# Optimization experiments

Measured on AMD Instinct MI355X. Metric: run time of the kernel, lower is better.

Reference implementation:

```python
import jax, jax.numpy as jnp
import numpy as np
import math

B, S, D, H = 2, 2048, 1024, 16
DH = D // H          # 64 head dim
BLK = 64             # SpargeAttn block size
TOPK = 0.5           # fraction of KV blocks kept per query block
NEG = -1e9


def setup_inputs() -> dict:
    key = jax.random.key(0)
    ks = jax.random.split(key, 8)
    s = 0.02
    return {
        "inputs": jax.random.normal(ks[0], (B, S, D), dtype=jnp.float32),
        "ln_g": jnp.ones((D,), jnp.float32),
        "ln_b": jnp.zeros((D,), jnp.float32),
        "Wq": jax.random.normal(ks[1], (D, D), jnp.float32) * s,
        "bq": jnp.zeros((D,), jnp.float32),
        "Wk": jax.random.normal(ks[2], (D, D), jnp.float32) * s,
        "bk": jnp.zeros((D,), jnp.float32),
        "Wv": jax.random.normal(ks[3], (D, D), jnp.float32) * s,
        "bv": jnp.zeros((D,), jnp.float32),
        "Wo": jax.random.normal(ks[4], (D, D), jnp.float32) * s,
        "bo": jnp.zeros((D,), jnp.float32),
    }


def _sparse_topk_attn(q, k, v):
    # q,k,v: [B,H,S,DH]. Block-mean-similarity top-k sparse causal attention
    # (SpargeAttn spas_sage2_attn_meansim_topk, fp32 reference semantics).
    nb = S // BLK
    qm = q.reshape(B, H, nb, BLK, DH).mean(3)          # [B,H,nb,DH]
    km = k.reshape(B, H, nb, BLK, DH).mean(3)
    sim = jnp.einsum('bhqd,bhkd->bhqk', qm, km)        # block similarity
    cblk = jnp.tril(jnp.ones((nb, nb), bool))          # causal block mask
    sim = jnp.where(cblk, sim, NEG)
    kk = max(1, int(math.ceil(TOPK * nb)))
    _, idx = jax.lax.top_k(sim, kk)                    # [B,H,nb,kk]
    blk = jax.nn.one_hot(idx, nb, dtype=jnp.float32).sum(-2) > 0  # [B,H,nb,nb]
    blk = (blk & cblk) | jnp.eye(nb, dtype=bool)       # keep diagonal block
    tok_mask = jnp.repeat(jnp.repeat(blk, BLK, axis=2), BLK, axis=3)  # [B,H,S,S]
    tok_mask = tok_mask & jnp.tril(jnp.ones((S, S), bool))
    scores = jnp.einsum('bhid,bhjd->bhij', q, k) / jnp.float32(math.sqrt(DH))
    scores = jnp.where(tok_mask, scores, NEG)
    p = jax.nn.softmax(scores, axis=-1)
    return jnp.einsum('bhij,bhjd->bhid', p, v)


def reference(inputs, ln_g, ln_b, Wq, bq, Wk, bk, Wv, bv, Wo, bo):
    # pre-norm LayerNorm
    mu = inputs.mean(-1, keepdims=True)
    var = inputs.var(-1, keepdims=True)
    x = (inputs - mu) * jax.lax.rsqrt(var + 1e-5) * ln_g + ln_b
    # QKV projections -> [B,H,S,DH]
    q = (x @ Wq + bq).reshape(B, S, H, DH).transpose(0, 2, 1, 3)
    k = (x @ Wk + bk).reshape(B, S, H, DH).transpose(0, 2, 1, 3)
    v = (x @ Wv + bv).reshape(B, S, H, DH).transpose(0, 2, 1, 3)
    ctx = _sparse_topk_attn(q, k, v)
    ctx = ctx.transpose(0, 2, 1, 3).reshape(B, S, D)
    return ctx @ Wo + bo
```

## Files before the change

kernel.cpp:

```cpp
#include <hip/hip_runtime.h>
#include <stdint.h>

#define DEV static __device__ __forceinline__

typedef __attribute__((ext_vector_type(8))) short s16x8;
typedef __attribute__((ext_vector_type(4))) float f32x4;

constexpr int Bdim = 2, Sdim = 2048, Ddim = 1024, Hdim = 16, DH = 64;
constexpr int Mrows = Bdim * Sdim;
constexpr int NB = 32;
constexpr int SEL_STRIDE = 18;

constexpr size_t OFF_XB    = 0;
constexpr size_t OFF_WTQKV = OFF_XB    + (size_t)Mrows*Ddim*2;
constexpr size_t OFF_WOT   = OFF_WTQKV + (size_t)3072*1024*2;
constexpr size_t OFF_QKV   = OFF_WOT   + (size_t)1024*1024*2;
constexpr size_t OFF_CTX   = OFF_QKV   + (size_t)Mrows*3072*2;
constexpr size_t OFF_XM    = OFF_CTX   + (size_t)Mrows*Ddim*2;
constexpr size_t OFF_QM    = OFF_XM    + (size_t)64*1024*4;
constexpr size_t OFF_KM    = OFF_QM    + (size_t)64*1024*4;
constexpr size_t OFF_BIASQ = OFF_KM    + (size_t)64*1024*4;
constexpr size_t OFF_SEL   = OFF_BIASQ + (size_t)3072*4;
constexpr size_t OFF_PART  = OFF_SEL   + (size_t)1024*SEL_STRIDE*4;

DEV float bf2f(unsigned short u){ union{unsigned int i; float f;} x; x.i = ((unsigned int)u)<<16; return x.f; }
DEV unsigned short f2bf(float f){ union{float f; unsigned int i;} x; x.f=f;
  unsigned int r = x.i + 0x7fffu + ((x.i>>16)&1u); return (unsigned short)(r>>16); }

DEV void gload16(const unsigned short* g, unsigned short* l){
  __builtin_amdgcn_global_load_lds(
      (__attribute__((address_space(1))) void*)(void*)g,
      (__attribute__((address_space(3))) void*)l, 16, 0, 0);
}

DEV float dppmax_step(float x, int v){ union{float f; int i;} a, b; a.f=x; b.i=v; return fmaxf(a.f,b.f); }
DEV float rowmax16(float x){
  union{float f; int i;} u;
  u.f = x; x = dppmax_step(x, __builtin_amdgcn_update_dpp(u.i,u.i,0xB1,0xF,0xF,true));
  u.f = x; x = dppmax_step(x, __builtin_amdgcn_update_dpp(u.i,u.i,0x4E,0xF,0xF,true));
  u.f = x; x = dppmax_step(x, __builtin_amdgcn_update_dpp(u.i,u.i,0x141,0xF,0xF,true));
  u.f = x; x = dppmax_step(x, __builtin_amdgcn_update_dpp(u.i,u.i,0x140,0xF,0xF,true));
  return x;
}

__global__ __launch_bounds__(256) void ln_kernel(const float* __restrict__ inp,
                                                 const float* __restrict__ gam,
                                                 const float* __restrict__ bet,
                                                 unsigned short* __restrict__ xb){
  const int row = blockIdx.x, t = threadIdx.x;
  __shared__ float red[8];
  const float4 v = ((const float4*)(inp + (size_t)row*Ddim))[t];
  float s  = v.x + v.y + v.z + v.w;
  float s2 = v.x*v.x + v.y*v.y + v.z*v.z + v.w*v.w;
#pragma unroll
  for (int mk=32; mk>=1; mk>>=1){ s += __shfl_xor(s, mk); s2 += __shfl_xor(s2, mk); }
  if ((t&63)==0){ red[t>>6] = s; red[4+(t>>6)] = s2; }
  __syncthreads();
  s  = red[0]+red[1]+red[2]+red[3];
  s2 = red[4]+red[5]+red[6]+red[7];
  const float mu  = s * (1.f/Ddim);
  const float var = s2 * (1.f/Ddim) - mu*mu;
  const float rs  = rsqrtf(var + 1e-5f);
  const float4 gv = ((const float4*)gam)[t];
  const float4 bv = ((const float4*)bet)[t];
  float o0 = (v.x-mu)*rs*gv.x + bv.x;
  float o1 = (v.y-mu)*rs*gv.y + bv.y;
  float o2 = (v.z-mu)*rs*gv.z + bv.z;
  float o3 = (v.w-mu)*rs*gv.w + bv.w;
  uint2 u;
  u.x = (unsigned int)f2bf(o0) | ((unsigned int)f2bf(o1)<<16);
  u.y = (unsigned int)f2bf(o2) | ((unsigned int)f2bf(o3)<<16);
  ((uint2*)(xb + (size_t)row*Ddim))[t] = u;
}

__global__ __launch_bounds__(256) void xm_kernel(const float* __restrict__ inp,
                                                 const float* __restrict__ gam,
                                                 const float* __restrict__ bet,
                                                 float* __restrict__ xm){
  const int blk = blockIdx.x, t = threadIdx.x;
  const int w = t>>6, lane = t&63;
  __shared__ float part[4][1024];
  float4 gv[4], bv[4];
#pragma unroll
  for (int p=0;p<4;++p){ gv[p] = ((const float4*)gam)[lane + 64*p];
                         bv[p] = ((const float4*)bet)[lane + 64*p]; }
  float ax[4][4];
#pragma unroll
  for (int p=0;p<4;++p)
#pragma unroll
    for (int c=0;c<4;++c) ax[p][c]=0.f;
  for (int rr=0; rr<16; ++rr){
    const int row = blk*64 + w*16 + rr;
    const float4* rp = (const float4*)(inp + (size_t)row*Ddim);
    float4 v[4]; float s=0.f, s2=0.f;
#pragma unroll
    for (int p=0;p<4;++p){
      v[p] = rp[lane + 64*p];
      s  += v[p].x+v[p].y+v[p].z+v[p].w;
      s2 += v[p].x*v[p].x+v[p].y*v[p].y+v[p].z*v[p].z+v[p].w*v[p].w;
    }
#pragma unroll
    for (int mk=32; mk>=1; mk>>=1){ s += __shfl_xor(s,mk); s2 += __shfl_xor(s2,mk); }
    const float mu = s*(1.f/Ddim);
    const float var = s2*(1.f/Ddim) - mu*mu;
    const float rs = rsqrtf(var + 1e-5f);
#pragma unroll
    for (int p=0;p<4;++p){
      ax[p][0] += (v[p].x-mu)*rs*gv[p].x + bv[p].x;
      ax[p][1] += (v[p].y-mu)*rs*gv[p].y + bv[p].y;
      ax[p][2] += (v[p].z-mu)*rs*gv[p].z + bv[p].z;
      ax[p][3] += (v[p].w-mu)*rs*gv[p].w + bv[p].w;
    }
  }
#pragma unroll
  for (int p=0;p<4;++p){
    float4 o; o.x=ax[p][0]; o.y=ax[p][1]; o.z=ax[p][2]; o.w=ax[p][3];
    ((float4*)&part[w][0])[lane + 64*p] = o;
  }
  __syncthreads();
  float4 r0 = ((float4*)&part[0][0])[t];
  float4 r1 = ((float4*)&part[1][0])[t];
  float4 r2 = ((float4*)&part[2][0])[t];
  float4 r3 = ((float4*)&part[3][0])[t];
  float4 o;
  o.x = (r0.x+r1.x+r2.x+r3.x)*(1.f/64);
  o.y = (r0.y+r1.y+r2.y+r3.y)*(1.f/64);
  o.z = (r0.z+r1.z+r2.z+r3.z)*(1.f/64);
  o.w = (r0.w+r1.w+r2.w+r3.w)*(1.f/64);
  ((float4*)(xm + (size_t)blk*Ddim))[t] = o;
}

__global__ __launch_bounds__(256) void wtrans4_kernel(const float* __restrict__ Wq,
                                                      const float* __restrict__ Wk,
                                                      const float* __restrict__ Wv,
                                                      const float* __restrict__ Wo,
                                                      unsigned short* __restrict__ wtqkv,
                                                      unsigned short* __restrict__ wot){
  __shared__ float tile[32][33];
  const int z = blockIdx.z;
  const float* W = (z==0)?Wq:(z==1)?Wk:(z==2)?Wv:Wo;
  unsigned short* Wt = (z<3) ? (wtqkv + (size_t)z*1024*1024) : wot;
  const int n0 = blockIdx.x*32, k0 = blockIdx.y*32;
  const int t = threadIdx.x, r = t>>5, c = t&31;
#pragma unroll
  for (int i=0;i<4;++i) tile[r+8*i][c] = W[(size_t)(k0 + r + 8*i)*1024 + n0 + c];
  __syncthreads();
#pragma unroll
  for (int i=0;i<4;++i) Wt[(size_t)(n0 + r + 8*i)*1024 + k0 + c] = f2bf(tile[c][r+8*i]);
}

__global__ void biascat_kernel(const float* __restrict__ bq, const float* __restrict__ bk,
                               const float* __restrict__ bv, float* __restrict__ outb){
  int i = blockIdx.x*256 + threadIdx.x;
  float v = (i<1024) ? bq[i] : (i<2048 ? bk[i-1024] : bv[i-2048]);
  outb[i] = v;
}

__global__ __launch_bounds__(256) void qmkm_part(const float* __restrict__ xm,
    const float* __restrict__ Wq, const float* __restrict__ Wk,
    float* __restrict__ part){
  const int c  = blockIdx.x*256 + threadIdx.x;
  const int rg = blockIdx.y >> 3, ks = blockIdx.y & 7;
  const int z  = blockIdx.z;
  const float* W = z ? Wk : Wq;
  const int r0 = rg*16, k0 = ks*128;
  float acc[16];
#pragma unroll
  for (int r=0;r<16;++r) acc[r]=0.f;
  for (int k=0;k<128;k+=4){
    const float wv0 = W[(size_t)(k0+k  )*1024 + c];
    const float wv1 = W[(size_t)(k0+k+1)*1024 + c];
    const float wv2 = W[(size_t)(k0+k+2)*1024 + c];
    const float wv3 = W[(size_t)(k0+k+3)*1024 + c];
#pragma unroll
    for (int r=0;r<16;++r){
      const float4 xv = *(const float4*)&xm[(size_t)(r0+r)*1024 + k0 + k];
      acc[r] = fmaf(xv.w, wv3, fmaf(xv.z, wv2, fmaf(xv.y, wv1, fmaf(xv.x, wv0, acc[r]))));
    }
  }
  float* dst = part + (((size_t)z*8 + ks)*64 + r0)*1024 + c;
#pragma unroll
  for (int r=0;r<16;++r) dst[(size_t)r*1024] = acc[r];
}

__global__ __launch_bounds__(256) void qmkm_reduce(const float* __restrict__ part,
    const float* __restrict__ bq, const float* __restrict__ bk,
    float* __restrict__ qm, float* __restrict__ km){
  const int idx = blockIdx.x*256 + threadIdx.x;
  const int z = blockIdx.y;
  const int c = idx & 1023, r = idx >> 10;
  const float* p = part + ((size_t)z*8*64*1024) + (size_t)r*1024 + c;
  float s = 0.f;
#pragma unroll
  for (int ks=0; ks<8; ++ks) s += p[(size_t)ks*64*1024];
  s += z ? bk[c] : bq[c];
  (z ? km : qm)[(size_t)r*1024 + c] = s;
}

__global__ __launch_bounds__(256) void topk_kernel(const float* __restrict__ qm,
                                                   const float* __restrict__ km,
                                                   int* __restrict__ sel){
  const int bhq = blockIdx.x;
  const int qb = bhq & 31, h = (bhq>>5) & 15, b = bhq >> 9;
  const int t = threadIdx.x;
  __shared__ float sim[32];
  __shared__ int keep[32];
  const int kb = t>>3, l8 = t&7;
  float acc = 0.f;
  if (kb <= qb){
    const float* qv = qm + (size_t)(b*32 + qb)*1024 + h*64;
    const float* kv = km + (size_t)(b*32 + kb)*1024 + h*64;
#pragma unroll
    for (int d=0; d<8; ++d) acc += qv[l8*8+d] * kv[l8*8+d];
  }
  acc += __shfl_xor(acc,1); acc += __shfl_xor(acc,2); acc += __shfl_xor(acc,4);
  if (l8==0) sim[kb] = (kb<=qb) ? acc : -1e30f;
  __syncthreads();
  if (t < 32){
    int k2 = t; int ok = 0;
    if (k2 <= qb){
      float sv = sim[k2]; int rank = 0;
      for (int j=0;j<=qb;++j){
        float sj = sim[j];
        rank += (sj > sv) || (sj == sv && j < k2);
      }
      ok = (rank < 16) || (k2 == qb);
    }
    keep[t] = ok;
  }
  __syncthreads();
  if (t == 0){
    int* dstp = sel + (size_t)bhq * SEL_STRIDE;
    int c = 0;
    for (int j=0;j<32;++j) if (keep[j]) dstp[1+c++] = j;
    dstp[0] = c;
  }
}

template<int OUT_BF16>
__global__ __launch_bounds__(256) void gemm_bt(const unsigned short* __restrict__ A,
                                               const unsigned short* __restrict__ Bt,
                                               const float* __restrict__ bias,
                                               void* __restrict__ C, int N){
  constexpr int K = 1024;
  __shared__ unsigned short ldsA[128*32];
  __shared__ unsigned short ldsB[128*32];
  const int t = threadIdx.x, lane = t & 63, wid = t >> 6;
  const int wr = wid >> 1, wc = wid & 1;
  const int rl = lane & 15, g = lane >> 4;

  const int nbx = gridDim.x;
  const int nwg = nbx * gridDim.y;
  const int id  = blockIdx.y * nbx + blockIdx.x;
  const int nid = (id & 7) * (nwg >> 3) + (id >> 3);
  const int m0 = (nid / nbx) * 128, n0 = (nid % nbx) * 128;

  const f32x4 ZERO4 = {0.f,0.f,0.f,0.f};
  f32x4 acc[4][4];
#pragma unroll
  for (int i=0;i<4;++i)
#pragma unroll
    for (int j=0;j<4;++j) acc[i][j] = ZERO4;

  const int slot0 = wid*128 + lane, slot1 = slot0 + 64;
  const int sr0 = slot0>>2, sc0 = slot0&3;
  const int sr1 = slot1>>2, sc1 = slot1&3;
  const unsigned short* A0 = A  + (size_t)(m0 + sr0)*K + (sc0 ^ ((sr0>>1)&3))*8;
  const unsigned short* A1 = A  + (size_t)(m0 + sr1)*K + (sc1 ^ ((sr1>>1)&3))*8;
  const unsigned short* B0 = Bt + (size_t)(n0 + sr0)*K + (sc0 ^ ((sr0>>1)&3))*8;
  const unsigned short* B1 = Bt + (size_t)(n0 + sr1)*K + (sc1 ^ ((sr1>>1)&3))*8;
  unsigned short* dA0 = ldsA + (wid*2+0)*512;
  unsigned short* dA1 = ldsA + (wid*2+1)*512;
  unsigned short* dB0 = ldsB + (wid*2+0)*512;
  unsigned short* dB1 = ldsB + (wid*2+1)*512;

  for (int k0=0; k0<K; k0+=32){
    __syncthreads();
    gload16(A0 + k0, dA0);
    gload16(A1 + k0, dA1);
    gload16(B0 + k0, dB0);
    gload16(B1 + k0, dB1);
    __syncthreads();
    s16x8 af[4], bfr[4];
#pragma unroll
    for (int mi=0;mi<4;++mi){
      int row = wr*64 + mi*16 + rl;
      af[mi] = *(const s16x8*)((char*)ldsA + row*64 + ((g ^ ((row>>1)&3))<<4));
    }
#pragma unroll
    for (int ni=0;ni<4;++ni){
      int row = wc*64 + ni*16 + rl;
      bfr[ni] = *(const s16x8*)((char*)ldsB + row*64 + ((g ^ ((row>>1)&3))<<4));
    }
#pragma unroll
    for (int mi=0;mi<4;++mi)
#pragma unroll
      for (int ni=0;ni<4;++ni)
        acc[mi][ni] = __builtin_amdgcn_mfma_f32_16x16x32_bf16(af[mi], bfr[ni], acc[mi][ni], 0,0,0);
  }

  const int r4 = g*4;
#pragma unroll
  for (int mi=0;mi<4;++mi){
#pragma unroll
    for (int ni=0;ni<4;++ni){
      int col = n0 + wc*64 + ni*16 + rl;
      float bb = bias[col];
#pragma unroll
      for (int e=0;e<4;++e){
        int row = m0 + wr*64 + mi*16 + r4 + e;
        float v = acc[mi][ni][e] + bb;
        if (OUT_BF16) ((unsigned short*)C)[(size_t)row*N + col] = f2bf(v);
        else          ((float*)C)[(size_t)row*N + col] = v;
      }
    }
  }
}

__global__ __launch_bounds__(256) void attn_kernel(const unsigned short* __restrict__ qkv,
                                                   const int* __restrict__ sel,
                                                   unsigned short* __restrict__ ctx){
  const int id = blockIdx.x;
  const int xcd = id & 7, jj = id >> 3;
  const int bh = xcd + 8*(jj/24);
  const int tau = jj % 24;
  const int h = bh & 15, b = bh >> 4;
  int qbl[2]; int nq;
  if (tau < 8){ qbl[0]=tau; qbl[1]=15-tau; nq=2; }
  else        { qbl[0]=tau+8; qbl[1]=0;    nq=1; }

  const int t = threadIdx.x, wid = t >> 6, lane = t & 63;
  const int rl = lane & 15, g = lane >> 4, r4 = g*4;

  __shared__ unsigned short K_s[2][64*64];
  __shared__ unsigned short V_s[2][80*64];
  __shared__ unsigned short P_s[4][16*64];

  for (int i=t; i<1024; i+=256){
    int r = 64 + (i>>6), c = i&63;
    unsigned short val = (r==64) ? (unsigned short)0x3F80 : (unsigned short)0;
    V_s[0][r*64+c] = val; V_s[1][r*64+c] = val;
  }

  const int jst = t >> 2, cq = t & 3;
  const unsigned short* kvbase = qkv + (size_t)(b*Sdim + jst)*3072 + h*DH;
  const int kwb0 = jst*128 + (((cq*2  ) ^ (jst&7))<<4);
  const int kwb1 = jst*128 + (((cq*2+1) ^ (jst&7))<<4);
  const f32x4 ZERO4 = {0.f,0.f,0.f,0.f};

  for (int iq=0; iq<nq; ++iq){
    const int qb = qbl[iq];
    const int* selrow = sel + (size_t)(((b*Hdim)+h)*NB + qb) * SEL_STRIDE;
    const int ns = selrow[0];

    const int qrow = b*Sdim + qb*64 + wid*16 + rl;
    const unsigned short* qbase = qkv + (size_t)qrow*3072 + h*DH;
    s16x8 qa[2];
#pragma unroll
    for (int kk=0; kk<2; ++kk){
      s16x8 raw = *(const s16x8*)(qbase + kk*32 + g*8);
      s16x8 qq;
#pragma unroll
      for (int e=0;e<8;++e) qq[e] = (short)f2bf(bf2f((unsigned short)raw[e]) * 0.125f);
      qa[kk] = qq;
    }

    f32x4 o[5];
    float m_r[4];
#pragma unroll
    for (int f=0; f<5; ++f) o[f] = ZERO4;
#pragma unroll
    for (int e=0;e<4;++e) m_r[e] = -3.0e38f;

    __syncthreads();

    int kb = selrow[1];
    s16x8 kr0, kr1, vr0, vr1;
    {
      const unsigned short* p = kvbase + (size_t)kb*64*3072;
      kr0 = *(const s16x8*)(p + 1024 + cq*16);
      kr1 = *(const s16x8*)(p + 1024 + cq*16 + 8);
      vr0 = *(const s16x8*)(p + 2048 + cq*16);
      vr1 = *(const s16x8*)(p + 2048 + cq*16 + 8);
    }

    for (int it=0; it<ns; ++it){
      const int buf = it & 1;
      unsigned short* Kw = &K_s[buf][0];
      unsigned short* Vw = &V_s[buf][0];
      *(s16x8*)((char*)Kw + kwb0) = kr0;
      *(s16x8*)((char*)Kw + kwb1) = kr1;
#pragma unroll
      for (int e=0;e<8;++e){
        int d1 = cq*16 + e, d2 = d1 + 8;
        int sw1 = (d1&7) ^ ((d1>>3)&7);
        int sw2 = (d2&7) ^ ((d2>>3)&7);
        *(unsigned short*)((char*)Vw + d1*128 + ((2*jst) ^ (sw1<<4))) = (unsigned short)vr0[e];
        *(unsigned short*)((char*)Vw + d2*128 + ((2*jst) ^ (sw2<<4))) = (unsigned short)vr1[e];
      }
      const int kbcur = kb;
      if (it+1 < ns){
        kb = selrow[2+it];
        const unsigned short* p = kvbase + (size_t)kb*64*3072;
        kr0 = *(const s16x8*)(p + 1024 + cq*16);
        kr1 = *(const s16x8*)(p + 1024 + cq*16 + 8);
        vr0 = *(const s16x8*)(p + 2048 + cq*16);
        vr1 = *(const s16x8*)(p + 2048 + cq*16 + 8);
      }
      __syncthreads();

      f32x4 sf[4];
#pragma unroll
      for (int f=0;f<4;++f) sf[f] = ZERO4;
#pragma unroll
      for (int kk=0;kk<2;++kk){
#pragma unroll
        for (int f=0;f<4;++f){
          int jr = f*16 + rl;
          s16x8 kf = *(const s16x8*)((char*)Kw + jr*128 + (((kk*4+g) ^ (jr&7))<<4));
          sf[f] = __builtin_amdgcn_mfma_f32_16x16x32_bf16(qa[kk], kf, sf[f], 0,0,0);
        }
      }
      if (kbcur == qb){
#pragma unroll
        for (int f=0;f<4;++f)
#pragma unroll
          for (int e=0;e<4;++e){
            int key = f*16 + rl;
            int qr  = wid*16 + r4 + e;
            if (key > qr) sf[f][e] = -1e9f;
          }
      }
      float alpha[4];
#pragma unroll
      for (int e=0;e<4;++e){
        float mx = fmaxf(fmaxf(sf[0][e], sf[1][e]), fmaxf(sf[2][e], sf[3][e]));
        mx = rowmax16(mx);
        float mn = fmaxf(m_r[e], mx);
        alpha[e] = __expf(m_r[e] - mn);
        m_r[e] = mn;
#pragma unroll
        for (int f=0;f<4;++f) sf[f][e] = __expf(sf[f][e] - mn);
      }
#pragma unroll
      for (int f=0;f<5;++f)
#pragma unroll
        for (int e=0;e<4;++e) o[f][e] = o[f][e] * alpha[e];

      char* Pw = (char*)&P_s[wid][0];
#pragma unroll
      for (int f=0;f<4;++f)
#pragma unroll
        for (int e=0;e<4;++e){
          int i_ = r4 + e;
          int sw = (i_&7) ^ (i_>>3);
          *(unsigned short*)(Pw + i_*128 + ((2*(f*16+rl)) ^ (sw<<4))) = f2bf(sf[f][e]);
        }

#pragma unroll
      for (int kk=0;kk<2;++kk){
        int swp = (rl&7) ^ (rl>>3);
        s16x8 pa = *(const s16x8*)(Pw + rl*128 + (((kk*4+g) ^ swp)<<4));
#pragma unroll
        for (int f=0;f<5;++f){
          int dr = f*16 + rl;
          int swv = (dr&7) ^ ((dr>>3)&7);
          s16x8 vf = *(const s16x8*)((char*)Vw + dr*128 + (((kk*4+g) ^ swv)<<4));
          o[f] = __builtin_amdgcn_mfma_f32_16x16x32_bf16(pa, vf, o[f], 0,0,0);
        }
      }
    }

    float l_e[4];
#pragma unroll
    for (int e=0;e<4;++e) l_e[e] = __shfl(o[4][e], lane & 48);
#pragma unroll
    for (int f=0;f<4;++f)
#pragma unroll
      for (int e=0;e<4;++e){
        int row = b*Sdim + qb*64 + wid*16 + r4 + e;
        int col = h*DH + f*16 + rl;
        ctx[(size_t)row*Ddim + col] = f2bf(o[f][e] / l_e[e]);
      }
  }
}

extern "C" void kernel_launch(void* const* d_in, const int* in_sizes, int n_in,
                              void* d_out, int out_size, void* d_ws, size_t ws_size,
                              hipStream_t stream){
  (void)in_sizes; (void)n_in; (void)out_size; (void)ws_size;
  const float* inp  = (const float*)d_in[0];
  const float* ln_g = (const float*)d_in[1];
  const float* ln_b = (const float*)d_in[2];
  const float* Wq   = (const float*)d_in[3];
  const float* bq   = (const float*)d_in[4];
  const float* Wk   = (const float*)d_in[5];
  const float* bk   = (const float*)d_in[6];
  const float* Wv   = (const float*)d_in[7];
  const float* bv   = (const float*)d_in[8];
  const float* Wo   = (const float*)d_in[9];
  const float* bo   = (const float*)d_in[10];

  char* ws = (char*)d_ws;
  unsigned short* xb    = (unsigned short*)(ws + OFF_XB);
  unsigned short* wtqkv = (unsigned short*)(ws + OFF_WTQKV);
  unsigned short* wot   = (unsigned short*)(ws + OFF_WOT);
  unsigned short* qkvb  = (unsigned short*)(ws + OFF_QKV);
  unsigned short* ctx   = (unsigned short*)(ws + OFF_CTX);
  float* xm   = (float*)(ws + OFF_XM);
  float* qm   = (float*)(ws + OFF_QM);
  float* km   = (float*)(ws + OFF_KM);
  float* bqkv = (float*)(ws + OFF_BIASQ);
  int*   sel  = (int*)(ws + OFF_SEL);
  float* part = (float*)(ws + OFF_PART);

  ln_kernel<<<Mrows, 256, 0, stream>>>(inp, ln_g, ln_b, xb);
  xm_kernel<<<64, 256, 0, stream>>>(inp, ln_g, ln_b, xm);
  wtrans4_kernel<<<dim3(32,32,4), 256, 0, stream>>>(Wq, Wk, Wv, Wo, wtqkv, wot);
  biascat_kernel<<<12, 256, 0, stream>>>(bq, bk, bv, bqkv);
  qmkm_part<<<dim3(4,32,2), 256, 0, stream>>>(xm, Wq, Wk, part);
  qmkm_reduce<<<dim3(256,2), 256, 0, stream>>>(part, bq, bk, qm, km);
  topk_kernel<<<1024, 256, 0, stream>>>(qm, km, sel);
  gemm_bt<1><<<dim3(24,32), 256, 0, stream>>>(xb, wtqkv, bqkv, (void*)qkvb, 3072);
  attn_kernel<<<768, 256, 0, stream>>>(qkvb, sel, ctx);
  gemm_bt<0><<<dim3(8,32), 256, 0, stream>>>(ctx, wot, bo, d_out, 1024);
}
```

Baseline: 164.2 us.

## Transpose attention score layout to keep P in registers; deepen GEMM K-tile

The attention kernel now computes S^T so that each lane holds one query row. Row max and sum then need only two cross-lane shuffles, and the softmax row sum is accumulated explicitly instead of through a ones-column in V. P is packed to bf16 with v_cvt_pk and redistributed through ds_bpermute rather than round-tripping through LDS, which removes the P_s buffer and the extra V column of MFMAs. Separately, the GEMM K-tile doubles to 64 with a new swizzle, halving barrier count per K, at the cost of more LDS per block.

```diff
diff --git a/kernel.cpp b/kernel.cpp
--- a/kernel.cpp
+++ b/kernel.cpp
@@ -33,14 +33,10 @@
       (__attribute__((address_space(3))) void*)l, 16, 0, 0);
 }
 
-DEV float dppmax_step(float x, int v){ union{float f; int i;} a, b; a.f=x; b.i=v; return fmaxf(a.f,b.f); }
-DEV float rowmax16(float x){
-  union{float f; int i;} u;
-  u.f = x; x = dppmax_step(x, __builtin_amdgcn_update_dpp(u.i,u.i,0xB1,0xF,0xF,true));
-  u.f = x; x = dppmax_step(x, __builtin_amdgcn_update_dpp(u.i,u.i,0x4E,0xF,0xF,true));
-  u.f = x; x = dppmax_step(x, __builtin_amdgcn_update_dpp(u.i,u.i,0x141,0xF,0xF,true));
-  u.f = x; x = dppmax_step(x, __builtin_amdgcn_update_dpp(u.i,u.i,0x140,0xF,0xF,true));
-  return x;
+DEV unsigned int cvtpk(float a, float b){
+  unsigned int r;
+  asm("v_cvt_pk_bf16_f32 %0, %1, %2" : "=v"(r) : "v"(a), "v"(b));
+  return r;
 }
 
 __global__ __launch_bounds__(256) void ln_kernel(const float* __restrict__ inp,
@@ -243,8 +239,8 @@
                                                const float* __restrict__ bias,
                                                void* __restrict__ C, int N){
   constexpr int K = 1024;
-  __shared__ unsigned short ldsA[128*32];
-  __shared__ unsigned short ldsB[128*32];
+  __shared__ unsigned short ldsA[128*64];
+  __shared__ unsigned short ldsB[128*64];
   const int t = threadIdx.x, lane = t & 63, wid = t >> 6;
   const int wr = wid >> 1, wc = wid & 1;
   const int rl = lane & 15, g = lane >> 4;
@@ -262,41 +258,42 @@
 #pragma unroll
     for (int j=0;j<4;++j) acc[i][j] = ZERO4;
 
-  const int slot0 = wid*128 + lane, slot1 = slot0 + 64;
-  const int sr0 = slot0>>2, sc0 = slot0&3;
-  const int sr1 = slot1>>2, sc1 = slot1&3;
-  const unsigned short* A0 = A  + (size_t)(m0 + sr0)*K + (sc0 ^ ((sr0>>1)&3))*8;
-  const unsigned short* A1 = A  + (size_t)(m0 + sr1)*K + (sc1 ^ ((sr1>>1)&3))*8;
-  const unsigned short* B0 = Bt + (size_t)(n0 + sr0)*K + (sc0 ^ ((sr0>>1)&3))*8;
-  const unsigned short* B1 = Bt + (size_t)(n0 + sr1)*K + (sc1 ^ ((sr1>>1)&3))*8;
-  unsigned short* dA0 = ldsA + (wid*2+0)*512;
-  unsigned short* dA1 = ldsA + (wid*2+1)*512;
-  unsigned short* dB0 = ldsB + (wid*2+0)*512;
-  unsigned short* dB1 = ldsB + (wid*2+1)*512;
-
-  for (int k0=0; k0<K; k0+=32){
+  const unsigned short* Ap[4]; const unsigned short* Bp[4];
+  unsigned short* dA[4]; unsigned short* dB[4];
+  const int csrc = (lane & 7) ^ (lane >> 3);
+#pragma unroll
+  for (int i=0;i<4;++i){
+    const int row_i = (wid*4+i)*8 + (lane>>3);
+    Ap[i] = A  + (size_t)(m0 + row_i)*K + csrc*8;
+    Bp[i] = Bt + (size_t)(n0 + row_i)*K + csrc*8;
+    dA[i] = ldsA + (wid*4+i)*512;
+    dB[i] = ldsB + (wid*4+i)*512;
+  }
+
+  for (int k0=0; k0<K; k0+=64){
     __syncthreads();
-    gload16(A0 + k0, dA0);
-    gload16(A1 + k0, dA1);
-    gload16(B0 + k0, dB0);
-    gload16(B1 + k0, dB1);
+#pragma unroll
+    for (int i=0;i<4;++i){ gload16(Ap[i] + k0, dA[i]); gload16(Bp[i] + k0, dB[i]); }
     __syncthreads();
-    s16x8 af[4], bfr[4];
-#pragma unroll
-    for (int mi=0;mi<4;++mi){
-      int row = wr*64 + mi*16 + rl;
-      af[mi] = *(const s16x8*)((char*)ldsA + row*64 + ((g ^ ((row>>1)&3))<<4));
-    }
-#pragma unroll
-    for (int ni=0;ni<4;++ni){
-      int row = wc*64 + ni*16 + rl;
-      bfr[ni] = *(const s16x8*)((char*)ldsB + row*64 + ((g ^ ((row>>1)&3))<<4));
-    }
-#pragma unroll
-    for (int mi=0;mi<4;++mi)
-#pragma unroll
-      for (int ni=0;ni<4;++ni)
-        acc[mi][ni] = __builtin_amdgcn_mfma_f32_16x16x32_bf16(af[mi], bfr[ni], acc[mi][ni], 0,0,0);
+#pragma unroll
+    for (int kk=0;kk<2;++kk){
+      s16x8 af[4], bfr[4];
+#pragma unroll
+      for (int mi=0;mi<4;++mi){
+        int row = wr*64 + mi*16 + rl;
+        af[mi] = *(const s16x8*)((char*)ldsA + row*128 + (((kk*4+g) ^ (rl&7))<<4));
+      }
+#pragma unroll
+      for (int ni=0;ni<4;++ni){
+        int row = wc*64 + ni*16 + rl;
+        bfr[ni] = *(const s16x8*)((char*)ldsB + row*128 + (((kk*4+g) ^ (rl&7))<<4));
+      }
+#pragma unroll
+      for (int mi=0;mi<4;++mi)
+#pragma unroll
+        for (int ni=0;ni<4;++ni)
+          acc[mi][ni] = __builtin_amdgcn_mfma_f32_16x16x32_bf16(af[mi], bfr[ni], acc[mi][ni], 0,0,0);
+    }
   }
 
   const int r4 = g*4;
@@ -330,31 +327,31 @@
   else        { qbl[0]=tau+8; qbl[1]=0;    nq=1; }
 
   const int t = threadIdx.x, wid = t >> 6, lane = t & 63;
-  const int rl = lane & 15, g = lane >> 4, r4 = g*4;
-
-  __shared__ unsigned short K_s[2][64*64];
-  __shared__ unsigned short V_s[2][80*64];
-  __shared__ unsigned short P_s[4][16*64];
-
-  for (int i=t; i<1024; i+=256){
-    int r = 64 + (i>>6), c = i&63;
-    unsigned short val = (r==64) ? (unsigned short)0x3F80 : (unsigned short)0;
-    V_s[0][r*64+c] = val; V_s[1][r*64+c] = val;
-  }
+  const int rl = lane & 15, g = lane >> 4;
+  const int q_local = wid*16 + rl;
+
+  __shared__ unsigned short K_s[2][4096];
+  __shared__ unsigned short V_s[2][4096];
 
   const int jst = t >> 2, cq = t & 3;
-  const unsigned short* kvbase = qkv + (size_t)(b*Sdim + jst)*3072 + h*DH;
+  const int r2 = t >> 3, dq = t & 7;
+  const unsigned short* kbase = qkv + (size_t)(b*Sdim + jst)*3072 + 1024 + h*DH + cq*16;
+  const unsigned short* vbase = qkv + (size_t)(b*Sdim + 2*r2)*3072 + 2048 + h*DH + dq*8;
   const int kwb0 = jst*128 + (((cq*2  ) ^ (jst&7))<<4);
   const int kwb1 = jst*128 + (((cq*2+1) ^ (jst&7))<<4);
   const f32x4 ZERO4 = {0.f,0.f,0.f,0.f};
+
+  const int src0 = (rl + 16*((2*g  ) & 3)) << 2;
+  const int src1 = (rl + 16*((2*g+1) & 3)) << 2;
+  const bool hsel = (g >> 1);
 
   for (int iq=0; iq<nq; ++iq){
     const int qb = qbl[iq];
     const int* selrow = sel + (size_t)(((b*Hdim)+h)*NB + qb) * SEL_STRIDE;
     const int ns = selrow[0];
 
-    const int qrow = b*Sdim + qb*64 + wid*16 + rl;
-    const unsigned short* qbase = qkv + (size_t)qrow*3072 + h*DH;
+    const int qg0 = b*Sdim + qb*64 + q_local;
+    const unsigned short* qbase = qkv + (size_t)qg0*3072 + h*DH;
     s16x8 qa[2];
 #pragma unroll
     for (int kk=0; kk<2; ++kk){
@@ -365,23 +362,21 @@
       qa[kk] = qq;
     }
 
-    f32x4 o[5];
-    float m_r[4];
-#pragma unroll
-    for (int f=0; f<5; ++f) o[f] = ZERO4;
-#pragma unroll
-    for (int e=0;e<4;++e) m_r[e] = -3.0e38f;
+    f32x4 o[4];
+    float m_r = -3.0e38f, l_r = 0.f;
+#pragma unroll
+    for (int f=0; f<4; ++f) o[f] = ZERO4;
 
     __syncthreads();
 
     int kb = selrow[1];
     s16x8 kr0, kr1, vr0, vr1;
     {
-      const unsigned short* p = kvbase + (size_t)kb*64*3072;
-      kr0 = *(const s16x8*)(p + 1024 + cq*16);
-      kr1 = *(const s16x8*)(p + 1024 + cq*16 + 8);
-      vr0 = *(const s16x8*)(p + 2048 + cq*16);
-      vr1 = *(const s16x8*)(p + 2048 + cq*16 + 8);
+      const size_t off = (size_t)kb*64*3072;
+      kr0 = *(const s16x8*)(kbase + off);
+      kr1 = *(const s16x8*)(kbase + off + 8);
+      vr0 = *(const s16x8*)(vbase + off);
+      vr1 = *(const s16x8*)(vbase + off + 3072);
     }
 
     for (int it=0; it<ns; ++it){
@@ -392,33 +387,33 @@
       *(s16x8*)((char*)Kw + kwb1) = kr1;
 #pragma unroll
       for (int e=0;e<8;++e){
-        int d1 = cq*16 + e, d2 = d1 + 8;
-        int sw1 = (d1&7) ^ ((d1>>3)&7);
-        int sw2 = (d2&7) ^ ((d2>>3)&7);
-        *(unsigned short*)((char*)Vw + d1*128 + ((2*jst) ^ (sw1<<4))) = (unsigned short)vr0[e];
-        *(unsigned short*)((char*)Vw + d2*128 + ((2*jst) ^ (sw2<<4))) = (unsigned short)vr1[e];
+        const int d1 = dq*8 + e;
+        const int sw = (d1&7) ^ (d1>>3);
+        const unsigned int pr = (unsigned int)(unsigned short)vr0[e]
+                              | ((unsigned int)(unsigned short)vr1[e] << 16);
+        *(unsigned int*)((char*)Vw + d1*128 + ((4*r2) ^ (sw<<4))) = pr;
       }
       const int kbcur = kb;
       if (it+1 < ns){
         kb = selrow[2+it];
-        const unsigned short* p = kvbase + (size_t)kb*64*3072;
-        kr0 = *(const s16x8*)(p + 1024 + cq*16);
-        kr1 = *(const s16x8*)(p + 1024 + cq*16 + 8);
-        vr0 = *(const s16x8*)(p + 2048 + cq*16);
-        vr1 = *(const s16x8*)(p + 2048 + cq*16 + 8);
+        const size_t off = (size_t)kb*64*3072;
+        kr0 = *(const s16x8*)(kbase + off);
+        kr1 = *(const s16x8*)(kbase + off + 8);
+        vr0 = *(const s16x8*)(vbase + off);
+        vr1 = *(const s16x8*)(vbase + off + 3072);
       }
       __syncthreads();
 
-      f32x4 sf[4];
-#pragma unroll
-      for (int f=0;f<4;++f) sf[f] = ZERO4;
+      f32x4 sfT[4];
+#pragma unroll
+      for (int f=0;f<4;++f) sfT[f] = ZERO4;
 #pragma unroll
       for (int kk=0;kk<2;++kk){
 #pragma unroll
         for (int f=0;f<4;++f){
-          int jr = f*16 + rl;
+          const int jr = f*16 + rl;
           s16x8 kf = *(const s16x8*)((char*)Kw + jr*128 + (((kk*4+g) ^ (jr&7))<<4));
-          sf[f] = __builtin_amdgcn_mfma_f32_16x16x32_bf16(qa[kk], kf, sf[f], 0,0,0);
+          sfT[f] = __builtin_amdgcn_mfma_f32_16x16x32_bf16(kf, qa[kk], sfT[f], 0,0,0);
         }
       }
       if (kbcur == qb){
@@ -426,62 +421,85 @@
         for (int f=0;f<4;++f)
 #pragma unroll
           for (int e=0;e<4;++e){
-            int key = f*16 + rl;
-            int qr  = wid*16 + r4 + e;
-            if (key > qr) sf[f][e] = -1e9f;
+            const int j = f*16 + g*4 + e;
+            if (j > q_local) sfT[f][e] = -1e9f;
           }
       }
-      float alpha[4];
-#pragma unroll
-      for (int e=0;e<4;++e){
-        float mx = fmaxf(fmaxf(sf[0][e], sf[1][e]), fmaxf(sf[2][e], sf[3][e]));
-        mx = rowmax16(mx);
-        float mn = fmaxf(m_r[e], mx);
-        alpha[e] = __expf(m_r[e] - mn);
-        m_r[e] = mn;
-#pragma unroll
-        for (int f=0;f<4;++f) sf[f][e] = __expf(sf[f][e] - mn);
-      }
-#pragma unroll
-      for (int f=0;f<5;++f)
-#pragma unroll
-        for (int e=0;e<4;++e) o[f][e] = o[f][e] * alpha[e];
-
-      char* Pw = (char*)&P_s[wid][0];
-#pragma unroll
-      for (int f=0;f<4;++f)
-#pragma unroll
-        for (int e=0;e<4;++e){
-          int i_ = r4 + e;
-          int sw = (i_&7) ^ (i_>>3);
-          *(unsigned short*)(Pw + i_*128 + ((2*(f*16+rl)) ^ (sw<<4))) = f2bf(sf[f][e]);
+      {
+        float mx = sfT[0][0];
+#pragma unroll
+        for (int f=0;f<4;++f)
+#pragma unroll
+          for (int e=0;e<4;++e) mx = fmaxf(mx, sfT[f][e]);
+        mx = fmaxf(mx, __shfl_xor(mx, 16));
+        mx = fmaxf(mx, __shfl_xor(mx, 32));
+        const float mn = fmaxf(m_r, mx);
+        const float al = __expf(m_r - mn);
+        m_r = mn;
+        float rs = 0.f;
+#pragma unroll
+        for (int f=0;f<4;++f)
+#pragma unroll
+          for (int e=0;e<4;++e){
+            const float p = __expf(sfT[f][e] - mn);
+            sfT[f][e] = p; rs += p;
+          }
+        rs += __shfl_xor(rs, 16);
+        rs += __shfl_xor(rs, 32);
+        l_r = l_r*al + rs;
+#pragma unroll
+        for (int f=0;f<4;++f)
+#pragma unroll
+          for (int e=0;e<4;++e) o[f][e] *= al;
+      }
+
+      unsigned int plo[4], phi[4];
+#pragma unroll
+      for (int f=0;f<4;++f){
+        plo[f] = cvtpk(sfT[f][0], sfT[f][1]);
+        phi[f] = cvtpk(sfT[f][2], sfT[f][3]);
+      }
+
+#pragma unroll
+      for (int kk=0;kk<2;++kk){
+        const int f0 = 2*kk, f1 = 2*kk+1;
+        unsigned int a0, b0, w0, w1, w2, w3;
+        a0 = __builtin_amdgcn_ds_bpermute(src0, plo[f0]);
+        b0 = __builtin_amdgcn_ds_bpermute(src0, plo[f1]);
+        w0 = hsel ? b0 : a0;
+        a0 = __builtin_amdgcn_ds_bpermute(src0, phi[f0]);
+        b0 = __builtin_amdgcn_ds_bpermute(src0, phi[f1]);
+        w1 = hsel ? b0 : a0;
+        a0 = __builtin_amdgcn_ds_bpermute(src1, plo[f0]);
+        b0 = __builtin_amdgcn_ds_bpermute(src1, plo[f1]);
+        w2 = hsel ? b0 : a0;
+        a0 = __builtin_amdgcn_ds_bpermute(src1, phi[f0]);
+        b0 = __builtin_amdgcn_ds_bpermute(src1, phi[f1]);
+        w3 = hsel ? b0 : a0;
+        union { unsigned int u[4]; s16x8 v; } pfc;
+        pfc.u[0] = w0; pfc.u[1] = w1; pfc.u[2] = w2; pfc.u[3] = w3;
+        const s16x8 pf = pfc.v;
+#pragma unroll
+        for (int f=0;f<4;++f){
+          const int d = f*16 + rl;
+          const int sw = (d&7) ^ (d>>3);
+          s16x8 vf = *(const s16x8*)((char*)Vw + d*128 + ((64*kk + 16*g) ^ (sw<<4)));
+          o[f] = __builtin_amdgcn_mfma_f32_16x16x32_bf16(vf, pf, o[f], 0,0,0);
         }
-
-#pragma unroll
-      for (int kk=0;kk<2;++kk){
-        int swp = (rl&7) ^ (rl>>3);
-        s16x8 pa = *(const s16x8*)(Pw + rl*128 + (((kk*4+g) ^ swp)<<4));
-#pragma unroll
-        for (int f=0;f<5;++f){
-          int dr = f*16 + rl;
-          int swv = (dr&7) ^ ((dr>>3)&7);
-          s16x8 vf = *(const s16x8*)((char*)Vw + dr*128 + (((kk*4+g) ^ swv)<<4));
-          o[f] = __builtin_amdgcn_mfma_f32_16x16x32_bf16(pa, vf, o[f], 0,0,0);
-        }
-      }
-    }
-
-    float l_e[4];
-#pragma unroll
-    for (int e=0;e<4;++e) l_e[e] = __shfl(o[4][e], lane & 48);
-#pragma unroll
-    for (int f=0;f<4;++f)
-#pragma unroll
-      for (int e=0;e<4;++e){
-        int row = b*Sdim + qb*64 + wid*16 + r4 + e;
-        int col = h*DH + f*16 + rl;
-        ctx[(size_t)row*Ddim + col] = f2bf(o[f][e] / l_e[e]);
-      }
+      }
+    }
+
+    {
+      const float inv = 1.f / l_r;
+      unsigned short* crow = ctx + (size_t)qg0*Ddim + h*DH;
+#pragma unroll
+      for (int f=0;f<4;++f){
+        uint2 st;
+        st.x = (unsigned int)f2bf(o[f][0]*inv) | ((unsigned int)f2bf(o[f][1]*inv)<<16);
+        st.y = (unsigned int)f2bf(o[f][2]*inv) | ((unsigned int)f2bf(o[f][3]*inv)<<16);
+        *(uint2*)(crow + f*16 + g*4) = st;
+      }
+    }
   }
 }
 
```

New measurement: 155.3 us. 1.06x faster.
